# Kernel optimization log

Measured on AMD Instinct MI355X. Metric: run time of the kernel, lower is better.

Reference implementation:

```python
import jax, jax.numpy as jnp
import numpy as np

# QMon (monDEQ, Winston & Kolter): conv pre-net -> MONSingleConv + MONBorderReLU solved
# with Peaceman-Rachford splitting -> border crop -> MLP head.
BATCH = 256
C = 64            # DEQ channels
N = 9             # DEQ spatial dim (in_dim=9)
K = 3             # MONSingleConv kernel size
M_STRONG = 0.1    # m (strong monotonicity)
ALPHA = 1.0
TOL = 1e-5
MAX_ITER = 50
OUT_FEATURES = 18


def conv2d(x, w, b=None, stride=1):
    y = jax.lax.conv_general_dilated(x, w, (stride, stride), 'VALID',
                                     dimension_numbers=('NCHW', 'OIHW', 'NCHW'))
    if b is not None:
        y = y + b[None, :, None, None]
    return y


def circ_conv(x, w, b=None):
    # circular-padded 'same' conv (cpad + valid conv in the torch code)
    p = (w.shape[2] - 1) // 2
    xp = jnp.pad(x, ((0, 0), (0, 0), (p, p), (p, p)), mode='wrap')
    return conv2d(xp, w, b)


def circ_conv_T(x, w):
    # adjoint of circular conv = circular conv with spatially-flipped, channel-transposed kernel
    wt = jnp.transpose(jnp.flip(w, (2, 3)), (1, 0, 2, 3))
    return circ_conv(x, wt)


def W_multiply(z, A_w, g):
    # W z = (1-m) z - g * A^T A z, with A Frobenius-normalized
    An = A_w / jnp.linalg.norm(A_w)
    Az = circ_conv(z, An)
    ATAz = circ_conv_T(Az, An)
    return (1.0 - M_STRONG) * z - g * ATAz


def build_inverse(A_w, g, n):
    # ((1+alpha) I - alpha W)^{-1} per 2D-DFT frequency (circular conv is block-circulant)
    An = A_w / jnp.linalg.norm(A_w)
    co, ci, k, _ = An.shape
    p = (k - 1) // 2
    kimg = jnp.zeros((co, ci, n, n), An.dtype)
    for dx in range(k):
        for dy in range(k):
            kimg = kimg.at[:, :, (dx - p) % n, (dy - p) % n].set(An[:, :, dx, dy])
    Af = jnp.conj(jnp.fft.fft2(kimg)).transpose(2, 3, 0, 1)  # (n,n,O,I): A_hat(w)
    I = jnp.eye(co, dtype=Af.dtype)
    c = (1.0 + ALPHA) - ALPHA * (1.0 - M_STRONG)
    Mmat = c * I + (ALPHA * g).astype(Af.dtype) * jnp.einsum('xyoi,xyoj->xyij', jnp.conj(Af), Af)
    return jnp.linalg.inv(Mmat)  # (n,n,C,C) complex


def apply_inverse(Vinv, z):
    zf = jnp.fft.fft2(z)                                  # (B,C,n,n)
    yf = jnp.einsum('xyoc,bcxy->boxy', Vinv, zf)
    return jnp.real(jnp.fft.ifft2(yf)).astype(z.dtype)


def mon_deq(xpre, U_w, U_b, A_w, g):
    n = xpre.shape[-1]
    bias = circ_conv(xpre, U_w, U_b)
    Vinv = build_inverse(A_w, g, n)
    mask = jnp.pad(jnp.ones((n - 2, n - 2), xpre.dtype), 1)[None, None]  # MONBorderReLU border=1
    brelu = lambda v: jax.nn.relu(v) * mask
    z0 = jnp.zeros_like(bias)

    def body(state):
        z, u, err, it = state
        u12 = 2.0 * z - u
        z12 = apply_inverse(Vinv, u12 + ALPHA * bias)
        un = 2.0 * z12 - u12
        zn = brelu(un)
        err = jnp.linalg.norm(zn - z) / (1e-6 + jnp.linalg.norm(zn))
        return zn, un, err, it + 1

    def cond(state):
        _, _, err, it = state
        return (err > TOL) & (it < MAX_ITER)

    z, u, err, it = jax.lax.while_loop(cond, body, (z0, z0, jnp.asarray(1.0, xpre.dtype), 0))
    # final pass with the linear operator (as in the torch forward after the no_grad solve)
    return brelu(W_multiply(z, A_w, g) + bias)


def setup_inputs() -> dict:
    key = jax.random.key(0)
    ks = jax.random.split(key, 12)

    def u(k, shape, fan_in):
        b = 1.0 / np.sqrt(fan_in)
        return jax.random.uniform(k, shape, jnp.float32, -b, b)

    x = jax.random.uniform(ks[0], (BATCH, 4, 84, 84), jnp.float32) * 255.0
    return dict(
        x=x,
        conv1_w=u(ks[1], (32, 4, 8, 8), 4 * 8 * 8), conv1_b=u(ks[2], (32,), 4 * 8 * 8),
        conv2_w=u(ks[3], (64, 32, 4, 4), 32 * 4 * 4), conv2_b=u(ks[4], (64,), 32 * 4 * 4),
        U_w=u(ks[5], (C, C, K, K), C * K * K), U_b=u(ks[6], (C,), C * K * K),
        A_w=u(ks[7], (C, C, K, K), C * K * K), g=jnp.asarray(1.0, jnp.float32),
        fc1_w=u(ks[8], (512, 3136), 3136), fc1_b=u(ks[9], (512,), 3136),
        fc2_w=u(ks[10], (OUT_FEATURES, 512), 512), fc2_b=u(ks[11], (OUT_FEATURES,), 512),
    )


def reference(x, conv1_w, conv1_b, conv2_w, conv2_b, U_w, U_b, A_w, g,
              fc1_w, fc1_b, fc2_w, fc2_b):
    h = jax.nn.relu(conv2d(x / 255.0, conv1_w, conv1_b, stride=4))   # (B,32,20,20)
    h = jax.nn.relu(conv2d(h, conv2_w, conv2_b, stride=2))           # (B,64,9,9)
    z = mon_deq(h, U_w, U_b, A_w, g)                                 # (B,64,9,9)
    z = z[:, :, 1:-1, 1:-1].reshape(z.shape[0], -1)                  # (B,3136)
    h = jax.nn.relu(z @ fc1_w.T + fc1_b)
    return h @ fc2_w.T + fc2_b
```

## Files before the change

### kernel.cpp

```cpp
#include <hip/hip_runtime.h>


#define NB 256
#define NCH 64
#define NP 81
#define NIMG (NB*NCH)
#define MAXIT 50
#define NCAN 41
#define CANON(l) ((l) < 5 ? (l) : (l) + 4)

constexpr float C9[9] = {
  1.0f, 0.76604444311897803f, 0.17364817766693041f, -0.5f,
  -0.93969262078590843f, -0.93969262078590843f, -0.5f,
  0.17364817766693041f, 0.76604444311897803f };
constexpr float S9[9] = {
  0.0f, 0.64278760968653936f, 0.98480775301220802f, 0.86602540378443871f,
  0.34202014332566877f, -0.34202014332566877f, -0.86602540378443871f,
  -0.98480775301220802f, -0.64278760968653936f };

__constant__ float COS9[9] = {
  1.0f, 0.76604444311897803f, 0.17364817766693041f, -0.5f,
  -0.93969262078590843f, -0.93969262078590843f, -0.5f,
  0.17364817766693041f, 0.76604444311897803f };
__constant__ float SIN9[9] = {
  0.0f, 0.64278760968653936f, 0.98480775301220802f, 0.86602540378443871f,
  0.34202014332566877f, -0.34202014332566877f, -0.86602540378443871f,
  -0.98480775301220802f, -0.64278760968653936f };

__global__ __launch_bounds__(256) void k_norm(const float* __restrict__ Aw,
                                              float* __restrict__ sc) {
    __shared__ float red[256];
    float s = 0.f;
    for (int i = threadIdx.x; i < 64*64*9; i += 256) { float a = Aw[i]; s += a*a; }
    red[threadIdx.x] = s; __syncthreads();
    for (int w = 128; w > 0; w >>= 1) {
        if (threadIdx.x < w) red[threadIdx.x] += red[threadIdx.x + w];
        __syncthreads();
    }
    if (threadIdx.x == 0) { float n = sqrtf(red[0]); sc[0] = n; sc[1] = 1.f/n; }
}

__global__ __launch_bounds__(512, 4) void k_conv1(const float* __restrict__ x,
                                                  const float* __restrict__ w,
                                                  const float* __restrict__ bb,
                                                  float* __restrict__ y) {
    __shared__ float xl[2*7056];
    int blk = blockIdx.x, tid = threadIdx.x;
    int b = blk >> 1, og = (blk & 1) << 4;
    float acc[16];
    #pragma unroll
    for (int o = 0; o < 16; ++o) acc[o] = 0.f;
    int p = tid, oy = p/20, ox = p%20;
    for (int cp = 0; cp < 2; ++cp) {
        __syncthreads();
        const float4* xg = (const float4*)(x + b*28224 + cp*14112);
        for (int i = tid; i < 3528; i += 512) ((float4*)xl)[i] = xg[i];
        __syncthreads();
        if (p < 400) {
            #pragma unroll
            for (int ci = 0; ci < 2; ++ci)
            #pragma unroll
            for (int ky = 0; ky < 8; ++ky) {
                const float* xr = xl + ci*7056 + (oy*4+ky)*84 + ox*4;
                float4 x0 = *(const float4*)xr;
                float4 x1 = *(const float4*)(xr+4);
                const float* wr = w + og*256 + (cp*2+ci)*64 + ky*8;
                #pragma unroll
                for (int o = 0; o < 16; ++o) {
                    const float* wo = wr + o*256;
                    acc[o] += x0.x*wo[0] + x0.y*wo[1] + x0.z*wo[2] + x0.w*wo[3]
                            + x1.x*wo[4] + x1.y*wo[5] + x1.z*wo[6] + x1.w*wo[7];
                }
            }
        }
    }
    if (p < 400) {
        #pragma unroll
        for (int o = 0; o < 16; ++o)
            y[b*12800 + (og+o)*400 + p] = fmaxf(acc[o]*(1.f/255.f) + bb[og+o], 0.f);
    }
}

__global__ __launch_bounds__(512, 4) void k_conv2(const float* __restrict__ h1,
                                                  const float* __restrict__ w2,
                                                  const float* __restrict__ b2,
                                                  float* __restrict__ h2) {
    int blk = blockIdx.x, tid = threadIdx.x;
    int b = blk >> 1, og = (blk & 1) << 5;
    __shared__ float hl[12800];
    for (int i = tid; i < 12800; i += 512) {
        int ci = i / 400, pix = i % 400, iy = pix / 20, ix = pix % 20;
        hl[ci*400 + ((iy&1)*2 + (ix&1))*100 + (iy>>1)*10 + (ix>>1)] = h1[b*12800 + i];
    }
    __syncthreads();
    for (int idx = tid; idx < 2592; idx += 512) {
        int o = og + idx/81, p = idx%81, oy = p/9, ox = p%9;
        float acc = 0.f;
        const float* wo = w2 + o*512;
        for (int ci = 0; ci < 32; ci++) {
            const float* base = hl + ci*400;
            const float* wb = wo + ci*16;
            #pragma unroll
            for (int ky = 0; ky < 4; ky++)
            #pragma unroll
            for (int kx = 0; kx < 4; kx++)
                acc += base[((ky&1)*2 + (kx&1))*100 + (oy + (ky>>1))*10 + (ox + (kx>>1))]
                     * wb[ky*4 + kx];
        }
        h2[b*5184 + o*81 + p] = fmaxf(acc + b2[o], 0.f);
    }
}

__global__ __launch_bounds__(512, 4) void k_bias(const float* __restrict__ h2,
                                                 const float* __restrict__ Uw,
                                                 const float* __restrict__ Ub,
                                                 float* __restrict__ bias) {
    int blk = blockIdx.x, tid = threadIdx.x;
    int b = blk >> 1, og = (blk & 1) << 5;
    __shared__ float h2l[5184];
    for (int i = tid; i < 5184; i += 512) h2l[i] = h2[b*5184 + i];
    __syncthreads();
    for (int idx = tid; idx < 2592; idx += 512) {
        int o = og + idx/81, p = idx%81, i0 = p/9, j0 = p%9;
        int im = (i0+8)%9, ip = (i0+1)%9, jm = (j0+8)%9, jp = (j0+1)%9;
        int r0 = im*9, r1 = i0*9, r2 = ip*9;
        float acc = 0.f;
        const float* wo = Uw + o*576;
        for (int ci = 0; ci < 64; ci++) {
            const float* hb = h2l + ci*81;
            const float* wb = wo + ci*9;
            acc += hb[r0+jm]*wb[0] + hb[r0+j0]*wb[1] + hb[r0+jp]*wb[2]
                 + hb[r1+jm]*wb[3] + hb[r1+j0]*wb[4] + hb[r1+jp]*wb[5]
                 + hb[r2+jm]*wb[6] + hb[r2+j0]*wb[7] + hb[r2+jp]*wb[8];
        }
        bias[b*5184 + o*81 + p] = acc + Ub[o];
    }
}

__global__ __launch_bounds__(256) void k_af(const float* __restrict__ Aw,
                                            const float* __restrict__ sc,
                                            float2* __restrict__ Af) {
    int l = blockIdx.x; int f = CANON(l);
    int x = f/9, y = f%9;
    float inv = sc[1];
    for (int pr = threadIdx.x; pr < 4096; pr += 256) {
        const float* a = Aw + pr*9;
        float re = 0.f, im = 0.f;
        #pragma unroll
        for (int dx = 0; dx < 3; dx++)
        #pragma unroll
        for (int dy = 0; dy < 3; dy++) {
            int tt = (x*(dx+8) + y*(dy+8)) % 9;
            float v = a[dx*3+dy] * inv;
            re += v * COS9[tt]; im += v * SIN9[tt];
        }
        Af[f*4096 + pr] = make_float2(re, im);
    }
}

__global__ __launch_bounds__(256) void k_mw(const float2* __restrict__ Af,
                                            const float* __restrict__ gp,
                                            float2* __restrict__ Mmat,
                                            float2* __restrict__ WmT) {
    int l = blockIdx.x; int f = CANON(l);
    float g = gp[0];
    __shared__ float2 Al[4096];
    for (int i = threadIdx.x; i < 4096; i += 256) Al[i] = Af[f*4096 + i];
    __syncthreads();
    for (int e = threadIdx.x; e < 4096; e += 256) {
        int i = e >> 6, j = e & 63;
        float sr = 0.f, si = 0.f;
        for (int o = 0; o < 64; o++) {
            float2 a = Al[o*64 + i], b = Al[o*64 + j];
            sr += a.x*b.x + a.y*b.y;
            si += a.x*b.y - a.y*b.x;
        }
        Mmat[f*4096 + e] = make_float2((i==j ? 1.1f : 0.f) + g*sr, g*si);
        WmT [f*4096 + j*64 + i] = make_float2((i==j ? 0.9f : 0.f) - g*sr, -g*si);
    }
}

__global__ __launch_bounds__(256) void k_inv(float2* __restrict__ Mio) {
    int l = blockIdx.x; int f = CANON(l);
    __shared__ float2 M[64*65];
    __shared__ float2 rowk[64];
    __shared__ float2 fcol[64];
    int tid = threadIdx.x;
    float2* Mg = Mio + f*4096;
    for (int e = tid; e < 4096; e += 256) M[(e>>6)*65 + (e&63)] = Mg[e];
    __syncthreads();
    int j = tid & 63, ig = tid >> 6;
    for (int k = 0; k < 64; k++) {
        if (ig == 0) {
            float2 d = M[k*65 + k];
            float den = 1.f / (d.x*d.x + d.y*d.y);
            float pr = d.x*den, pi = -d.y*den;
            float2 m = M[k*65 + j];
            rowk[j] = (j == k) ? make_float2(pr, pi)
                               : make_float2(m.x*pr - m.y*pi, m.x*pi + m.y*pr);
        } else if (ig == 1) {
            fcol[j] = M[j*65 + k];
        }
        __syncthreads();
        #pragma unroll 4
        for (int s = 0; s < 16; s++) {
            int i = (ig << 4) + s;
            if (i == k) {
                M[i*65 + j] = rowk[j];
            } else {
                float2 fi = fcol[i];
                if (j == k) {
                    float2 rk = rowk[k];
                    M[i*65 + j] = make_float2(-(fi.x*rk.x - fi.y*rk.y),
                                              -(fi.x*rk.y + fi.y*rk.x));
                } else {
                    float2 r = rowk[j]; float2 m = M[i*65 + j];
                    M[i*65 + j] = make_float2(m.x - (fi.x*r.x - fi.y*r.y),
                                              m.y - (fi.x*r.y + fi.y*r.x));
                }
            }
        }
        __syncthreads();
    }
    for (int e = tid; e < 4096; e += 256) {
        int i2 = e >> 6, j2 = e & 63;
        Mio[f*4096 + j2*64 + i2] = M[i2*65 + j2];
    }
}

__global__ __launch_bounds__(192) void k_fft(const float* __restrict__ in,
                                             float2* __restrict__ Tf) {
    __shared__ float2 T1[16*83];
    int tid = threadIdx.x;
    int img = tid & 15, j = tid >> 4;
    int gimg = blockIdx.x*16 + img;
    if (j < 9) {
        int r = j;
        float tn[9];
        const float* gp = in + gimg*81 + r*9;
        #pragma unroll
        for (int xc = 0; xc < 9; ++xc) tn[xc] = gp[xc];
        #pragma unroll
        for (int ky = 0; ky < 9; ++ky) {
            float sr = 0.f, si = 0.f;
            #pragma unroll
            for (int xx = 0; xx < 9; ++xx) {
                const int m = (ky*xx) % 9;
                sr += tn[xx]*C9[m];
                si -= tn[xx]*S9[m];
            }
            T1[img*83 + r*9 + ky] = make_float2(sr, si);
        }
    }
    __syncthreads();
    if (j < 9) {
        int ky = j;
        float2 s[9];
        #pragma unroll
        for (int r = 0; r < 9; ++r) s[r] = T1[img*83 + r*9 + ky];
        #pragma unroll
        for (int kx = 0; kx < 5; ++kx) {
            float fr = 0.f, fi = 0.f;
            #pragma unroll
            for (int r = 0; r < 9; ++r) {
                const int m = (kx*r) % 9;
                fr += s[r].x*C9[m] + s[r].y*S9[m];
                fi += s[r].y*C9[m] - s[r].x*S9[m];
            }
            if (kx > 0 || ky < 5)
                Tf[(kx*9 + ky)*NIMG + gimg] = make_float2(fr, fi);
        }
    }
}

__global__ __launch_bounds__(256) void k_mv(const float2* __restrict__ Tf,
                                            float2* __restrict__ Yf,
                                            const float2* __restrict__ V) {
    int l = blockIdx.x >> 4, bc = blockIdx.x & 15;
    int f = CANON(l);
    int lane = threadIdx.x & 63;
    int wid  = __builtin_amdgcn_readfirstlane((int)(threadIdx.x >> 6));
    int b0 = bc*16 + wid*4;
    const float2* Vg = V + f*4096 + lane;
    const float2* Tg = Tf + f*NIMG + b0*64;
    float2 a0 = make_float2(0.f,0.f), a1 = a0, a2 = a0, a3 = a0;
    #pragma unroll 8
    for (int c = 0; c < 64; ++c) {
        float2 v = Vg[c*64];
        float2 t0 = Tg[c], t1 = Tg[64+c], t2 = Tg[128+c], t3 = Tg[192+c];
        a0.x += v.x*t0.x - v.y*t0.y; a0.y += v.x*t0.y + v.y*t0.x;
        a1.x += v.x*t1.x - v.y*t1.y; a1.y += v.x*t1.y + v.y*t1.x;
        a2.x += v.x*t2.x - v.y*t2.y; a2.y += v.x*t2.y + v.y*t2.x;
        a3.x += v.x*t3.x - v.y*t3.y; a3.y += v.x*t3.y + v.y*t3.x;
    }
    float2* Yg = Yf + f*NIMG + b0*64 + lane;
    Yg[0] = a0; Yg[64] = a1; Yg[128] = a2; Yg[192] = a3;
}

__global__ __launch_bounds__(192) void k_fuse(const float2* __restrict__ Yf,
                                              float* __restrict__ u12g,
                                              const float* __restrict__ bias,
                                              float2* __restrict__ Tf,
                                              int last) {
    __shared__ float2 T1[16*83];
    int tid = threadIdx.x;
    int img = tid & 15, j = tid >> 4;
    int gimg = blockIdx.x*16 + img;
    if (j < 9) {
        int ky = j;
        float2 y[9];
        #pragma unroll
        for (int kx = 0; kx < 9; ++kx) {
            int fc; bool cj;
            if (kx == 0)      { cj = (ky >= 5); fc = cj ? (9 - ky) : ky; }
            else if (kx <= 4) { cj = false;     fc = kx*9 + ky; }
            else              { cj = true;      fc = (9-kx)*9 + (ky ? 9-ky : 0); }
            float2 a = Yf[fc*NIMG + gimg];
            y[kx] = make_float2(a.x, cj ? -a.y : a.y);
        }
        #pragma unroll
        for (int r = 0; r < 9; ++r) {
            float sr = 0.f, si = 0.f;
            #pragma unroll
            for (int kx = 0; kx < 9; ++kx) {
                const int m = (r*kx) % 9;
                sr += y[kx].x*C9[m] - y[kx].y*S9[m];
                si += y[kx].x*S9[m] + y[kx].y*C9[m];
            }
            T1[img*83 + r*9 + ky] = make_float2(sr, si);
        }
    }
    __syncthreads();
    if (j < 9) {
        int r = j;
        float2 t1[9];
        #pragma unroll
        for (int ky = 0; ky < 9; ++ky) t1[ky] = T1[img*83 + r*9 + ky];
        float tn[9];
        int gb = gimg*81 + r*9;
        #pragma unroll
        for (int xc = 0; xc < 9; ++xc) {
            float yr = 0.f;
            #pragma unroll
            for (int ky = 0; ky < 9; ++ky) {
                const int m = (xc*ky) % 9;
                yr += t1[ky].x*C9[m] - t1[ky].y*S9[m];
            }
            yr *= (1.f/81.f);
            float u12v = u12g[gb + xc];
            float un = 2.f*yr - u12v;
            bool interior = (r >= 1 && r <= 7 && xc >= 1 && xc <= 7);
            float zn = interior ? fmaxf(un, 0.f) : 0.f;
            float u12n = 2.f*zn - un;
            u12g[gb + xc] = u12n;
            tn[xc] = last ? zn : (u12n + bias[gb + xc]);
        }
        #pragma unroll
        for (int ky = 0; ky < 9; ++ky) {
            float sr = 0.f, si = 0.f;
            #pragma unroll
            for (int xx = 0; xx < 9; ++xx) {
                const int m = (ky*xx) % 9;
                sr += tn[xx]*C9[m];
                si -= tn[xx]*S9[m];
            }
            T1[img*83 + r*9 + ky] = make_float2(sr, si);
        }
    }
    __syncthreads();
    if (j < 9) {
        int ky = j;
        float2 s[9];
        #pragma unroll
        for (int r = 0; r < 9; ++r) s[r] = T1[img*83 + r*9 + ky];
        #pragma unroll
        for (int kx = 0; kx < 5; ++kx) {
            float fr = 0.f, fi = 0.f;
            #pragma unroll
            for (int r = 0; r < 9; ++r) {
                const int m = (kx*r) % 9;
                fr += s[r].x*C9[m] + s[r].y*S9[m];
                fi += s[r].y*C9[m] - s[r].x*S9[m];
            }
            if (kx > 0 || ky < 5)
                Tf[(kx*9 + ky)*NIMG + gimg] = make_float2(fr, fi);
        }
    }
}

__global__ __launch_bounds__(192) void k_crop(const float2* __restrict__ Yf,
                                              const float* __restrict__ bias,
                                              float* __restrict__ zc) {
    __shared__ float2 T1[16*83];
    int tid = threadIdx.x;
    int img = tid & 15, j = tid >> 4;
    int gimg = blockIdx.x*16 + img;
    if (j < 9) {
        int ky = j;
        float2 y[9];
        #pragma unroll
        for (int kx = 0; kx < 9; ++kx) {
            int fc; bool cj;
            if (kx == 0)      { cj = (ky >= 5); fc = cj ? (9 - ky) : ky; }
            else if (kx <= 4) { cj = false;     fc = kx*9 + ky; }
            else              { cj = true;      fc = (9-kx)*9 + (ky ? 9-ky : 0); }
            float2 a = Yf[fc*NIMG + gimg];
            y[kx] = make_float2(a.x, cj ? -a.y : a.y);
        }
        #pragma unroll
        for (int r = 0; r < 9; ++r) {
            float sr = 0.f, si = 0.f;
            #pragma unroll
            for (int kx = 0; kx < 9; ++kx) {
                const int m = (r*kx) % 9;
                sr += y[kx].x*C9[m] - y[kx].y*S9[m];
                si += y[kx].x*S9[m] + y[kx].y*C9[m];
            }
            T1[img*83 + r*9 + ky] = make_float2(sr, si);
        }
    }
    __syncthreads();
    if (j >= 1 && j <= 7) {
        int r = j;
        float2 t1[9];
        #pragma unroll
        for (int ky = 0; ky < 9; ++ky) t1[ky] = T1[img*83 + r*9 + ky];
        int gb = gimg*81 + r*9;
        float* zr = zc + (gimg >> 6)*3136 + (gimg & 63)*49 + (r-1)*7;
        #pragma unroll
        for (int xc = 1; xc < 8; ++xc) {
            float yr = 0.f;
            #pragma unroll
            for (int ky = 0; ky < 9; ++ky) {
                const int m = (xc*ky) % 9;
                yr += t1[ky].x*C9[m] - t1[ky].y*S9[m];
            }
            yr *= (1.f/81.f);
            zr[xc-1] = fmaxf(yr + bias[gb + xc], 0.f);
        }
    }
}

__global__ __launch_bounds__(256) void k_fc1(const float* __restrict__ A,
                                             const float* __restrict__ W,
                                             const float* __restrict__ bb,
                                             float* __restrict__ H) {
    int bt = blockIdx.x >> 5, ot = blockIdx.x & 31;
    int b0 = bt*16, o0 = ot*16;
    __shared__ float At[16][65], Bt[16][65];
    int tid = threadIdx.x;
    int row = tid >> 6, col = tid & 63;
    int tb = tid >> 4, to = tid & 15;
    float acc = 0.f;
    for (int k0 = 0; k0 < 3136; k0 += 64) {
        #pragma unroll
        for (int s = 0; s < 4; s++) {
            int rr = row + s*4;
            At[rr][col] = A[(b0+rr)*3136 + k0 + col];
            Bt[rr][col] = W[(o0+rr)*3136 + k0 + col];
        }
        __syncthreads();
        #pragma unroll
        for (int kk = 0; kk < 64; kk++)
            acc += At[tb][kk] * Bt[to][kk];
        __syncthreads();
    }
    H[(b0+tb)*512 + o0+to] = fmaxf(acc + bb[o0+to], 0.f);
}

__global__ __launch_bounds__(256) void k_fc2(const float* __restrict__ H,
                                             const float* __restrict__ W,
                                             const float* __restrict__ bb,
                                             float* __restrict__ out) {
    int idx = blockIdx.x*256 + threadIdx.x;
    if (idx >= 4608) return;
    int b = idx/18, o = idx%18;
    const float* h = H + b*512;
    const float* w = W + o*512;
    float acc = 0.f;
    for (int k = 0; k < 512; k++) acc += h[k]*w[k];
    out[idx] = acc + bb[o];
}

extern "C" void kernel_launch(void* const* d_in, const int* in_sizes, int n_in,
                              void* d_out, int out_size, void* d_ws, size_t ws_size,
                              hipStream_t stream) {
    (void)in_sizes; (void)n_in; (void)out_size; (void)ws_size;
    const float* x   = (const float*)d_in[0];
    const float* c1w = (const float*)d_in[1];
    const float* c1b = (const float*)d_in[2];
    const float* c2w = (const float*)d_in[3];
    const float* c2b = (const float*)d_in[4];
    const float* Uw  = (const float*)d_in[5];
    const float* Ub  = (const float*)d_in[6];
    const float* Aw  = (const float*)d_in[7];
    const float* gp  = (const float*)d_in[8];
    const float* f1w = (const float*)d_in[9];
    const float* f1b = (const float*)d_in[10];
    const float* f2w = (const float*)d_in[11];
    const float* f2b = (const float*)d_in[12];

    float* ws = (float*)d_ws;
    float*  h1   = ws + 0;
    float2* Tf   = (float2*)(ws + 0);
    float*  bias = ws + 3276800;
    float*  u12  = ws + 4603904;
    float2* Yf   = (float2*)(ws + 5931008);
    float2* Af   = (float2*)(ws + 8585216);
    float2* Minv = (float2*)(ws + 9248768);
    float2* WmT  = (float2*)(ws + 9912320);
    float*  zc   = ws + 10575872;
    float*  hfc  = ws + 11378688;
    float*  sc   = ws + 11509760;
    float*  h2   = ws + 11509764;

    hipMemsetAsync(u12, 0, (size_t)1327104*sizeof(float), stream);

    k_norm <<<1,   256, 0, stream>>>(Aw, sc);
    k_conv1<<<512, 512, 0, stream>>>(x, c1w, c1b, h1);
    k_conv2<<<512, 512, 0, stream>>>(h1, c2w, c2b, h2);
    k_bias <<<512, 512, 0, stream>>>(h2, Uw, Ub, bias);
    k_af   <<<NCAN,256, 0, stream>>>(Aw, sc, Af);
    k_mw   <<<NCAN,256, 0, stream>>>(Af, gp, Minv, WmT);
    k_inv  <<<NCAN,256, 0, stream>>>(Minv);

    k_fft<<<1024,192,0,stream>>>(bias, Tf);
    for (int it = 0; it < MAXIT; it++) {
        k_mv  <<<NCAN*16,256,0,stream>>>(Tf, Yf, Minv);
        k_fuse<<<1024,   192,0,stream>>>(Yf, u12, bias, Tf, it == MAXIT-1);
    }
    k_mv  <<<NCAN*16,256,0,stream>>>(Tf, Yf, WmT);
    k_crop<<<1024,   192,0,stream>>>(Yf, bias, zc);

    k_fc1<<<512,256,0,stream>>>(zc, f1w, f1b, hfc);
    k_fc2<<<18, 256,0,stream>>>(hfc, f2w, f2b, (float*)d_out);
}
```

Before: 1.956 ms.

## Transpose bias/u12 to pixel-major layout and rework FFT kernels for coalescing

The bias and u12 state buffers are stored pixel-major (pixel, image) instead of image-major, so the FFT, fuse and crop kernels can read and write them with coalesced per-lane accesses. Those kernels now use 64 images per block with one wave per row or column and no idle threads, and their shared memory is laid out so lanes index consecutive words. k_bias stages its output through shared memory to write the transposed layout. k_inv is rewritten as a single-wave Gauss-Jordan that uses wave barriers instead of block-wide syncs, which serializes its row updates across one wave.

```diff
diff --git a/kernel.cpp b/kernel.cpp
--- a/kernel.cpp
+++ b/kernel.cpp
@@ -114,14 +114,15 @@
 __global__ __launch_bounds__(512, 4) void k_bias(const float* __restrict__ h2,
                                                  const float* __restrict__ Uw,
                                                  const float* __restrict__ Ub,
-                                                 float* __restrict__ bias) {
+                                                 float* __restrict__ biasT) {
     int blk = blockIdx.x, tid = threadIdx.x;
     int b = blk >> 1, og = (blk & 1) << 5;
     __shared__ float h2l[5184];
+    __shared__ float bt[2592];
     for (int i = tid; i < 5184; i += 512) h2l[i] = h2[b*5184 + i];
     __syncthreads();
     for (int idx = tid; idx < 2592; idx += 512) {
-        int o = og + idx/81, p = idx%81, i0 = p/9, j0 = p%9;
+        int oc = idx/81, o = og + oc, p = idx%81, i0 = p/9, j0 = p%9;
         int im = (i0+8)%9, ip = (i0+1)%9, jm = (j0+8)%9, jp = (j0+1)%9;
         int r0 = im*9, r1 = i0*9, r2 = ip*9;
         float acc = 0.f;
@@ -133,7 +134,12 @@
                  + hb[r1+jm]*wb[3] + hb[r1+j0]*wb[4] + hb[r1+jp]*wb[5]
                  + hb[r2+jm]*wb[6] + hb[r2+j0]*wb[7] + hb[r2+jp]*wb[8];
         }
-        bias[b*5184 + o*81 + p] = acc + Ub[o];
+        bt[oc*81 + p] = acc + Ub[o];
+    }
+    __syncthreads();
+    for (int idx = tid; idx < 2592; idx += 512) {
+        int p = idx >> 5, o32 = idx & 31;
+        biasT[p*NIMG + b*64 + og + o32] = bt[o32*81 + p];
     }
 }
 
@@ -180,66 +186,49 @@
     }
 }
 
-__global__ __launch_bounds__(256) void k_inv(float2* __restrict__ Mio) {
-    int l = blockIdx.x; int f = CANON(l);
+__global__ __launch_bounds__(64) void k_inv(float2* __restrict__ Mio) {
+    int f = CANON((int)blockIdx.x);
     __shared__ float2 M[64*65];
-    __shared__ float2 rowk[64];
-    __shared__ float2 fcol[64];
-    int tid = threadIdx.x;
+    int j = threadIdx.x;
     float2* Mg = Mio + f*4096;
-    for (int e = tid; e < 4096; e += 256) M[(e>>6)*65 + (e&63)] = Mg[e];
-    __syncthreads();
-    int j = tid & 63, ig = tid >> 6;
-    for (int k = 0; k < 64; k++) {
-        if (ig == 0) {
-            float2 d = M[k*65 + k];
-            float den = 1.f / (d.x*d.x + d.y*d.y);
-            float pr = d.x*den, pi = -d.y*den;
-            float2 m = M[k*65 + j];
-            rowk[j] = (j == k) ? make_float2(pr, pi)
-                               : make_float2(m.x*pr - m.y*pi, m.x*pi + m.y*pr);
-        } else if (ig == 1) {
-            fcol[j] = M[j*65 + k];
-        }
-        __syncthreads();
+    for (int i = 0; i < 64; ++i) M[i*65 + j] = Mg[i*64 + j];
+    __builtin_amdgcn_wave_barrier();
+    for (int k = 0; k < 64; ++k) {
+        float2 d = M[k*65 + k];
+        float den = 1.f / (d.x*d.x + d.y*d.y);
+        float pr = d.x*den, pi = -d.y*den;
+        float2 mk = M[k*65 + j];
+        float2 rkj = (j == k) ? make_float2(pr, pi)
+                              : make_float2(mk.x*pr - mk.y*pi, mk.x*pi + mk.y*pr);
+        __builtin_amdgcn_wave_barrier();
         #pragma unroll 4
-        for (int s = 0; s < 16; s++) {
-            int i = (ig << 4) + s;
-            if (i == k) {
-                M[i*65 + j] = rowk[j];
-            } else {
-                float2 fi = fcol[i];
-                if (j == k) {
-                    float2 rk = rowk[k];
-                    M[i*65 + j] = make_float2(-(fi.x*rk.x - fi.y*rk.y),
-                                              -(fi.x*rk.y + fi.y*rk.x));
-                } else {
-                    float2 r = rowk[j]; float2 m = M[i*65 + j];
-                    M[i*65 + j] = make_float2(m.x - (fi.x*r.x - fi.y*r.y),
-                                              m.y - (fi.x*r.y + fi.y*r.x));
-                }
-            }
-        }
-        __syncthreads();
-    }
-    for (int e = tid; e < 4096; e += 256) {
-        int i2 = e >> 6, j2 = e & 63;
-        Mio[f*4096 + j2*64 + i2] = M[i2*65 + j2];
-    }
-}
-
-__global__ __launch_bounds__(192) void k_fft(const float* __restrict__ in,
+        for (int i = 0; i < 64; ++i) {
+            float2 fi  = M[i*65 + k];
+            float2 cur = M[i*65 + j];
+            float2 nv;
+            if (i == k)      nv = rkj;
+            else if (j == k) nv = make_float2(-(fi.x*pr - fi.y*pi),
+                                              -(fi.x*pi + fi.y*pr));
+            else             nv = make_float2(cur.x - (fi.x*rkj.x - fi.y*rkj.y),
+                                              cur.y - (fi.x*rkj.y + fi.y*rkj.x));
+            __builtin_amdgcn_wave_barrier();
+            M[i*65 + j] = nv;
+            __builtin_amdgcn_wave_barrier();
+        }
+    }
+    for (int c = 0; c < 64; ++c) Mg[c*64 + j] = M[j*65 + c];
+}
+
+__global__ __launch_bounds__(576) void k_fft(const float* __restrict__ biasT,
                                              float2* __restrict__ Tf) {
-    __shared__ float2 T1[16*83];
-    int tid = threadIdx.x;
-    int img = tid & 15, j = tid >> 4;
-    int gimg = blockIdx.x*16 + img;
-    if (j < 9) {
+    __shared__ float2 T1[81*64];
+    int lane = threadIdx.x & 63, j = threadIdx.x >> 6;
+    int gimg = blockIdx.x*64 + lane;
+    {
         int r = j;
         float tn[9];
-        const float* gp = in + gimg*81 + r*9;
-        #pragma unroll
-        for (int xc = 0; xc < 9; ++xc) tn[xc] = gp[xc];
+        #pragma unroll
+        for (int xc = 0; xc < 9; ++xc) tn[xc] = biasT[(r*9 + xc)*NIMG + gimg];
         #pragma unroll
         for (int ky = 0; ky < 9; ++ky) {
             float sr = 0.f, si = 0.f;
@@ -249,15 +238,15 @@
                 sr += tn[xx]*C9[m];
                 si -= tn[xx]*S9[m];
             }
-            T1[img*83 + r*9 + ky] = make_float2(sr, si);
-        }
-    }
-    __syncthreads();
-    if (j < 9) {
+            T1[(r*9 + ky)*64 + lane] = make_float2(sr, si);
+        }
+    }
+    __syncthreads();
+    {
         int ky = j;
         float2 s[9];
         #pragma unroll
-        for (int r = 0; r < 9; ++r) s[r] = T1[img*83 + r*9 + ky];
+        for (int r = 0; r < 9; ++r) s[r] = T1[(r*9 + ky)*64 + lane];
         #pragma unroll
         for (int kx = 0; kx < 5; ++kx) {
             float fr = 0.f, fi = 0.f;
@@ -297,16 +286,15 @@
     Yg[0] = a0; Yg[64] = a1; Yg[128] = a2; Yg[192] = a3;
 }
 
-__global__ __launch_bounds__(192) void k_fuse(const float2* __restrict__ Yf,
-                                              float* __restrict__ u12g,
-                                              const float* __restrict__ bias,
+__global__ __launch_bounds__(576) void k_fuse(const float2* __restrict__ Yf,
+                                              float* __restrict__ u12T,
+                                              const float* __restrict__ biasT,
                                               float2* __restrict__ Tf,
                                               int last) {
-    __shared__ float2 T1[16*83];
-    int tid = threadIdx.x;
-    int img = tid & 15, j = tid >> 4;
-    int gimg = blockIdx.x*16 + img;
-    if (j < 9) {
+    __shared__ float2 T1[81*64];
+    int lane = threadIdx.x & 63, j = threadIdx.x >> 6;
+    int gimg = blockIdx.x*64 + lane;
+    {
         int ky = j;
         float2 y[9];
         #pragma unroll
@@ -327,17 +315,16 @@
                 sr += y[kx].x*C9[m] - y[kx].y*S9[m];
                 si += y[kx].x*S9[m] + y[kx].y*C9[m];
             }
-            T1[img*83 + r*9 + ky] = make_float2(sr, si);
-        }
-    }
-    __syncthreads();
-    if (j < 9) {
+            T1[(r*9 + ky)*64 + lane] = make_float2(sr, si);
+        }
+    }
+    __syncthreads();
+    {
         int r = j;
         float2 t1[9];
         #pragma unroll
-        for (int ky = 0; ky < 9; ++ky) t1[ky] = T1[img*83 + r*9 + ky];
+        for (int ky = 0; ky < 9; ++ky) t1[ky] = T1[(r*9 + ky)*64 + lane];
         float tn[9];
-        int gb = gimg*81 + r*9;
         #pragma unroll
         for (int xc = 0; xc < 9; ++xc) {
             float yr = 0.f;
@@ -347,13 +334,14 @@
                 yr += t1[ky].x*C9[m] - t1[ky].y*S9[m];
             }
             yr *= (1.f/81.f);
-            float u12v = u12g[gb + xc];
+            int gi = (r*9 + xc)*NIMG + gimg;
+            float u12v = u12T[gi];
             float un = 2.f*yr - u12v;
             bool interior = (r >= 1 && r <= 7 && xc >= 1 && xc <= 7);
             float zn = interior ? fmaxf(un, 0.f) : 0.f;
             float u12n = 2.f*zn - un;
-            u12g[gb + xc] = u12n;
-            tn[xc] = last ? zn : (u12n + bias[gb + xc]);
+            u12T[gi] = u12n;
+            tn[xc] = last ? zn : (u12n + biasT[gi]);
         }
         #pragma unroll
         for (int ky = 0; ky < 9; ++ky) {
@@ -364,15 +352,15 @@
                 sr += tn[xx]*C9[m];
                 si -= tn[xx]*S9[m];
             }
-            T1[img*83 + r*9 + ky] = make_float2(sr, si);
-        }
-    }
-    __syncthreads();
-    if (j < 9) {
+            T1[(r*9 + ky)*64 + lane] = make_float2(sr, si);
+        }
+    }
+    __syncthreads();
+    {
         int ky = j;
         float2 s[9];
         #pragma unroll
-        for (int r = 0; r < 9; ++r) s[r] = T1[img*83 + r*9 + ky];
+        for (int r = 0; r < 9; ++r) s[r] = T1[(r*9 + ky)*64 + lane];
         #pragma unroll
         for (int kx = 0; kx < 5; ++kx) {
             float fr = 0.f, fi = 0.f;
@@ -388,14 +376,13 @@
     }
 }
 
-__global__ __launch_bounds__(192) void k_crop(const float2* __restrict__ Yf,
-                                              const float* __restrict__ bias,
+__global__ __launch_bounds__(576) void k_crop(const float2* __restrict__ Yf,
+                                              const float* __restrict__ biasT,
                                               float* __restrict__ zc) {
-    __shared__ float2 T1[16*83];
-    int tid = threadIdx.x;
-    int img = tid & 15, j = tid >> 4;
-    int gimg = blockIdx.x*16 + img;
-    if (j < 9) {
+    __shared__ float2 T1[81*64];
+    int lane = threadIdx.x & 63, j = threadIdx.x >> 6;
+    int gimg = blockIdx.x*64 + lane;
+    {
         int ky = j;
         float2 y[9];
         #pragma unroll
@@ -416,7 +403,7 @@
                 sr += y[kx].x*C9[m] - y[kx].y*S9[m];
                 si += y[kx].x*S9[m] + y[kx].y*C9[m];
             }
-            T1[img*83 + r*9 + ky] = make_float2(sr, si);
+            T1[(r*9 + ky)*64 + lane] = make_float2(sr, si);
         }
     }
     __syncthreads();
@@ -424,8 +411,7 @@
         int r = j;
         float2 t1[9];
         #pragma unroll
-        for (int ky = 0; ky < 9; ++ky) t1[ky] = T1[img*83 + r*9 + ky];
-        int gb = gimg*81 + r*9;
+        for (int ky = 0; ky < 9; ++ky) t1[ky] = T1[(r*9 + ky)*64 + lane];
         float* zr = zc + (gimg >> 6)*3136 + (gimg & 63)*49 + (r-1)*7;
         #pragma unroll
         for (int xc = 1; xc < 8; ++xc) {
@@ -436,7 +422,7 @@
                 yr += t1[ky].x*C9[m] - t1[ky].y*S9[m];
             }
             yr *= (1.f/81.f);
-            zr[xc-1] = fmaxf(yr + bias[gb + xc], 0.f);
+            zr[xc-1] = fmaxf(yr + biasT[(r*9 + xc)*NIMG + gimg], 0.f);
         }
     }
 }
@@ -501,37 +487,37 @@
     const float* f2b = (const float*)d_in[12];
 
     float* ws = (float*)d_ws;
-    float*  h1   = ws + 0;
-    float2* Tf   = (float2*)(ws + 0);
-    float*  bias = ws + 3276800;
-    float*  u12  = ws + 4603904;
-    float2* Yf   = (float2*)(ws + 5931008);
-    float2* Af   = (float2*)(ws + 8585216);
-    float2* Minv = (float2*)(ws + 9248768);
-    float2* WmT  = (float2*)(ws + 9912320);
-    float*  zc   = ws + 10575872;
-    float*  hfc  = ws + 11378688;
-    float*  sc   = ws + 11509760;
-    float*  h2   = ws + 11509764;
-
-    hipMemsetAsync(u12, 0, (size_t)1327104*sizeof(float), stream);
+    float*  h1    = ws + 0;
+    float2* Tf    = (float2*)(ws + 0);
+    float*  biasT = ws + 3276800;
+    float*  u12T  = ws + 4603904;
+    float2* Yf    = (float2*)(ws + 5931008);
+    float2* Af    = (float2*)(ws + 8585216);
+    float2* Minv  = (float2*)(ws + 9248768);
+    float2* WmT   = (float2*)(ws + 9912320);
+    float*  zc    = ws + 10575872;
+    float*  hfc   = ws + 11378688;
+    float*  sc    = ws + 11509760;
+    float*  h2    = ws + 11509764;
+
+    hipMemsetAsync(u12T, 0, (size_t)1327104*sizeof(float), stream);
 
     k_norm <<<1,   256, 0, stream>>>(Aw, sc);
     k_conv1<<<512, 512, 0, stream>>>(x, c1w, c1b, h1);
     k_conv2<<<512, 512, 0, stream>>>(h1, c2w, c2b, h2);
-    k_bias <<<512, 512, 0, stream>>>(h2, Uw, Ub, bias);
+    k_bias <<<512, 512, 0, stream>>>(h2, Uw, Ub, biasT);
     k_af   <<<NCAN,256, 0, stream>>>(Aw, sc, Af);
     k_mw   <<<NCAN,256, 0, stream>>>(Af, gp, Minv, WmT);
-    k_inv  <<<NCAN,256, 0, stream>>>(Minv);
-
-    k_fft<<<1024,192,0,stream>>>(bias, Tf);
+    k_inv  <<<NCAN,64,  0, stream>>>(Minv);
+
+    k_fft<<<256, 576, 0, stream>>>(biasT, Tf);
     for (int it = 0; it < MAXIT; it++) {
-        k_mv  <<<NCAN*16,256,0,stream>>>(Tf, Yf, Minv);
-        k_fuse<<<1024,   192,0,stream>>>(Yf, u12, bias, Tf, it == MAXIT-1);
-    }
-    k_mv  <<<NCAN*16,256,0,stream>>>(Tf, Yf, WmT);
-    k_crop<<<1024,   192,0,stream>>>(Yf, bias, zc);
-
-    k_fc1<<<512,256,0,stream>>>(zc, f1w, f1b, hfc);
-    k_fc2<<<18, 256,0,stream>>>(hfc, f2w, f2b, (float*)d_out);
-}
+        k_mv  <<<NCAN*16, 256, 0, stream>>>(Tf, Yf, Minv);
+        k_fuse<<<256,     576, 0, stream>>>(Yf, u12T, biasT, Tf, it == MAXIT-1);
+    }
+    k_mv  <<<NCAN*16, 256, 0, stream>>>(Tf, Yf, WmT);
+    k_crop<<<256,     576, 0, stream>>>(Yf, biasT, zc);
+
+    k_fc1<<<512, 256, 0, stream>>>(zc, f1w, f1b, hfc);
+    k_fc2<<<18,  256, 0, stream>>>(hfc, f2w, f2b, (float*)d_out);
+}
```

After: 2.086 ms. 1.07x slower.
